# Kernel optimization log

Measured on AMD Instinct MI355X. Metric: run time of the kernel, lower is better.

Reference implementation:

```python
import jax, jax.numpy as jnp
import numpy as np

B, S, D, E, TOP_K = 4, 4096, 2048, 64, 2

def setup_inputs() -> dict:
    key = jax.random.key(0)
    k1, k2, k3, k4 = jax.random.split(key, 4)
    return {
        "mh_output": jax.random.normal(k1, (B, S, D), dtype=jnp.float32),
        "W_route": jax.random.normal(k2, (D, E), dtype=jnp.float32) * (1.0 / np.sqrt(D)),
        "b_route": jnp.zeros((E,), dtype=jnp.float32),
        "W_noise": jax.random.normal(k3, (D, E), dtype=jnp.float32) * (1.0 / np.sqrt(D)),
        "b_noise": jnp.zeros((E,), dtype=jnp.float32),
        "noise": jax.random.normal(k4, (B, S, E), dtype=jnp.float32),
    }

def reference(mh_output, W_route, b_route, W_noise, b_noise, noise):
    # logits / noise logits: [B, S, E]
    logits = jnp.einsum("bsd,de->bse", mh_output, W_route) + b_route
    noise_logits = jnp.einsum("bsd,de->bse", mh_output, W_noise) + b_noise
    noisy_logits = logits + noise * jax.nn.softplus(noise_logits)

    top_vals, indices = jax.lax.top_k(noisy_logits, TOP_K)  # [B,S,K]

    # scatter top-k values into a -inf-filled tensor, then softmax
    flat_vals = top_vals.reshape(-1, TOP_K)
    flat_idx = indices.reshape(-1, TOP_K)
    n_tok = flat_idx.shape[0]
    rows = jnp.arange(n_tok)[:, None]
    sparse = jnp.full((n_tok, E), -jnp.inf, dtype=noisy_logits.dtype)
    sparse = sparse.at[rows, flat_idx].set(flat_vals)
    probs = jax.nn.softmax(sparse, axis=-1).reshape(noisy_logits.shape)
    return probs, indices
```

## Files before the change

### kernel.cpp

```cpp
#include <hip/hip_runtime.h>
#include <math.h>

#define M_TOK 16384
#define D_DIM 2048
#define E_EXP 64
#define NCOL  128
#define BM    64
#define BK    64
#define NITER (D_DIM / BK)

typedef float  f32x4  __attribute__((ext_vector_type(4)));
typedef short  bf16x8 __attribute__((ext_vector_type(8)));

#define MFMA_B16(a, b, c) __builtin_amdgcn_mfma_f32_16x16x32_bf16((a), (b), (c), 0, 0, 0)

__device__ __forceinline__ unsigned short bfrne(float f) {
    unsigned int u = __float_as_uint(f);
    return (unsigned short)((u + 0x7fffu + ((u >> 16) & 1u)) >> 16);
}
__device__ __forceinline__ float bfhi(unsigned short h) {
    return __uint_as_float((unsigned int)h << 16);
}

__device__ __forceinline__ bool beats(double va, int ia, double vb, int ib) {
    return (va > vb) || (va == vb && ia < ib);
}

__device__ __forceinline__ void gload16(const void* g, void* lds) {
    __builtin_amdgcn_global_load_lds(
        (const __attribute__((address_space(1))) unsigned int*)g,
        (__attribute__((address_space(3))) unsigned int*)lds, 16, 0, 0);
}

__global__ __launch_bounds__(256) void prep_w(
    const float* __restrict__ Wr, const float* __restrict__ Wn,
    unsigned short* __restrict__ Wg)
{
    const int g    = blockIdx.x * 256 + threadIdx.x;
    const int lane = g & 63;
    const int cf   = (g >> 6) & 7;
    const int kblk = g >> 9;
    const int colL = (cf & 3) * 16 + (lane & 15);
    const float* __restrict__ W = (cf < 4) ? Wr : Wn;
    const int kbase = kblk * 32 + (lane >> 4) * 8;

    bf16x8 o0, o1, o2;
    #pragma unroll
    for (int j = 0; j < 8; ++j) {
        const float w = W[(size_t)(kbase + j) * E_EXP + colL];
        const unsigned short h0 = bfrne(w);
        const float r  = w - bfhi(h0);
        const unsigned short h1 = bfrne(r);
        const float r2 = r - bfhi(h1);
        const unsigned short h2 = bfrne(r2);
        o0[j] = (short)h0; o1[j] = (short)h1; o2[j] = (short)h2;
    }
    const size_t s0 = (((size_t)kblk * 3 + 0) * 8 + cf) * 64 + lane;
    const size_t s1 = (((size_t)kblk * 3 + 1) * 8 + cf) * 64 + lane;
    const size_t s2 = (((size_t)kblk * 3 + 2) * 8 + cf) * 64 + lane;
    *(bf16x8*)(Wg + s0 * 8) = o0;
    *(bf16x8*)(Wg + s1 * 8) = o1;
    *(bf16x8*)(Wg + s2 * 8) = o2;
}

__device__ __forceinline__ void load_b(const unsigned short* __restrict__ Wg,
                                       int it, int wc, int lane,
                                       bf16x8 (&Bv)[2][2][3])
{
    #pragma unroll
    for (int s = 0; s < 2; ++s) {
        const int kblk = it * 2 + s;
        #pragma unroll
        for (int cfi = 0; cfi < 2; ++cfi) {
            #pragma unroll
            for (int p = 0; p < 3; ++p) {
                const size_t idx = (((size_t)kblk * 3 + p) * 8 + (wc * 2 + cfi)) * 64 + lane;
                Bv[s][cfi][p] = *(const bf16x8*)(Wg + idx * 8);
            }
        }
    }
}

__device__ __forceinline__ void stage_a(const float* __restrict__ A, float* Alds,
                                        int buf, int k0, int tokBase, int tid)
{
    #pragma unroll
    for (int i = 0; i < 2; ++i) {
        const int c    = i * 512 + tid;
        const int tok  = c >> 4;
        const int off  = (c & 15) * 16;
        const int soff = off ^ ((tok & 7) << 4);
        const float* g = A + (size_t)(tokBase + tok) * D_DIM + k0 + (soff >> 2);
        char* l = (char*)Alds + buf * (BM * BK * 4) + i * 8192 + (tid >> 6) * 1024;
        gload16(g, l);
    }
}

__device__ __forceinline__ void split8(const float4& a, const float4& b,
                                       bf16x8& o0, bf16x8& o1, bf16x8& o2)
{
    const float v[8] = {a.x, a.y, a.z, a.w, b.x, b.y, b.z, b.w};
    #pragma unroll
    for (int j = 0; j < 8; ++j) {
        const unsigned short h0 = bfrne(v[j]);
        const float r  = v[j] - bfhi(h0);
        const unsigned short h1 = bfrne(r);
        const float r2 = r - bfhi(h1);
        const unsigned short h2 = bfrne(r2);
        o0[j] = (short)h0; o1[j] = (short)h1; o2[j] = (short)h2;
    }
}

__device__ __forceinline__ void compute_iter(const float* Abuf, int wr, int wc, int lane,
                                             const bf16x8 (&Bc)[2][2][3],
                                             f32x4 (&acch)[2][2], f32x4 (&accl)[2][2])
{
    const char* Ab = (const char*)Abuf;
    #pragma unroll
    for (int s = 0; s < 2; ++s) {
        bf16x8 a0[2], a1[2], a2[2];
        #pragma unroll
        for (int rf = 0; rf < 2; ++rf) {
            const int row  = wr * 32 + rf * 16 + (lane & 15);
            const int base = row * 256 + s * 128 + (lane >> 4) * 32;
            const int sw   = (row & 7) << 4;
            const float4 p = *(const float4*)(Ab + (base ^ sw));
            const float4 q = *(const float4*)(Ab + ((base + 16) ^ sw));
            split8(p, q, a0[rf], a1[rf], a2[rf]);
        }
        #pragma unroll
        for (int cfi = 0; cfi < 2; ++cfi) {
            #pragma unroll
            for (int rf = 0; rf < 2; ++rf) {
                acch[rf][cfi] = MFMA_B16(a0[rf], Bc[s][cfi][0], acch[rf][cfi]);
                accl[rf][cfi] = MFMA_B16(a0[rf], Bc[s][cfi][1], accl[rf][cfi]);
                accl[rf][cfi] = MFMA_B16(a1[rf], Bc[s][cfi][0], accl[rf][cfi]);
                accl[rf][cfi] = MFMA_B16(a1[rf], Bc[s][cfi][1], accl[rf][cfi]);
                accl[rf][cfi] = MFMA_B16(a0[rf], Bc[s][cfi][2], accl[rf][cfi]);
                accl[rf][cfi] = MFMA_B16(a2[rf], Bc[s][cfi][0], accl[rf][cfi]);
            }
        }
    }
}

__global__ __launch_bounds__(512, 2) void fused_router(
    const float* __restrict__ A,
    const unsigned short* __restrict__ Wg,
    const float* __restrict__ br, const float* __restrict__ bn,
    const float* __restrict__ noise,
    float* __restrict__ probs, float* __restrict__ idxo)
{
    __shared__ float Alds[2 * BM * BK];
    __shared__ float Llds[BM][NCOL + 1];

    const int tid  = threadIdx.x;
    const int lane = tid & 63;
    const int wid  = tid >> 6;
    const int wr   = wid >> 2;
    const int wc   = wid & 3;
    const int tokBase = blockIdx.x * BM;

    f32x4 acch[2][2], accl[2][2];
    const f32x4 zero4 = {0.f, 0.f, 0.f, 0.f};
    #pragma unroll
    for (int a = 0; a < 2; ++a)
        #pragma unroll
        for (int b = 0; b < 2; ++b) { acch[a][b] = zero4; accl[a][b] = zero4; }

    bf16x8 B0[2][2][3], B1[2][2][3];
    load_b(Wg, 0, wc, lane, B0);
    stage_a(A, Alds, 0, 0, tokBase, tid);
    asm volatile("s_waitcnt vmcnt(0)" ::: "memory");
    __syncthreads();

    #pragma unroll 1
    for (int it2 = 0; it2 < NITER / 2; ++it2) {
        const int ita = it2 * 2;
        const int itb = ita + 1;
        load_b(Wg, itb, wc, lane, B1);
        stage_a(A, Alds, 1, itb * BK, tokBase, tid);
        compute_iter(Alds, wr, wc, lane, B0, acch, accl);
        asm volatile("s_waitcnt vmcnt(0)" ::: "memory");
        __syncthreads();
        if (itb + 1 < NITER) {
            load_b(Wg, itb + 1, wc, lane, B0);
            stage_a(A, Alds, 0, (itb + 1) * BK, tokBase, tid);
        }
        compute_iter(Alds + BM * BK, wr, wc, lane, B1, acch, accl);
        asm volatile("s_waitcnt vmcnt(0)" ::: "memory");
        __syncthreads();
    }

    #pragma unroll
    for (int rf = 0; rf < 2; ++rf) {
        #pragma unroll
        for (int cfi = 0; cfi < 2; ++cfi) {
            const int col  = wc * 32 + cfi * 16 + (lane & 15);
            const int rowb = wr * 32 + rf * 16 + (lane >> 4) * 4;
            #pragma unroll
            for (int r = 0; r < 4; ++r)
                Llds[rowb + r][col] = acch[rf][cfi][r] + accl[rf][cfi][r];
        }
    }
    __syncthreads();

    const int token = tid >> 3;
    const int s8    = tid & 7;
    const int tokG  = tokBase + token;

    double v0 = -INFINITY, v1 = -INFINITY;
    int i0 = 0, i1 = 0;
    const float* nz = noise + (size_t)tokG * E_EXP + s8 * 8;
    #pragma unroll
    for (int j = 0; j < 8; ++j) {
        const int e = s8 * 8 + j;
        const double lg = (double)Llds[token][e]      + (double)br[e];
        const double nl = (double)Llds[token][64 + e] + (double)bn[e];
        const double sp = fmax(nl, 0.0) + log1p(exp(-fabs(nl)));
        const double v  = fma((double)nz[j], sp, lg);
        if (beats(v, e, v0, i0))      { v1 = v0; i1 = i0; v0 = v; i0 = e; }
        else if (beats(v, e, v1, i1)) { v1 = v;  i1 = e; }
    }
    #pragma unroll
    for (int m = 1; m < 8; m <<= 1) {
        const double w0 = __shfl_xor(v0, m), w1 = __shfl_xor(v1, m);
        const int    j0 = __shfl_xor(i0, m), j1 = __shfl_xor(i1, m);
        if (beats(v0, i0, w0, j0)) {
            if (!beats(v1, i1, w0, j0)) { v1 = w0; i1 = j0; }
        } else {
            if (beats(v0, i0, w1, j1)) { v1 = v0; i1 = i0; }
            else                       { v1 = w1; i1 = j1; }
            v0 = w0; i0 = j0;
        }
    }
    const double e1  = exp(v1 - v0);
    const double den = 1.0 + e1;
    const float p0 = (float)(1.0 / den);
    const float p1 = (float)(e1 / den);

    float out[8];
    #pragma unroll
    for (int j = 0; j < 8; ++j) {
        const int e = s8 * 8 + j;
        out[j] = (e == i0) ? p0 : ((e == i1) ? p1 : 0.0f);
    }
    float* pb = probs + (size_t)tokG * E_EXP + s8 * 8;
    *(float4*)(pb)     = make_float4(out[0], out[1], out[2], out[3]);
    *(float4*)(pb + 4) = make_float4(out[4], out[5], out[6], out[7]);
    if (s8 == 0)
        *(float2*)(idxo + (size_t)tokG * 2) = make_float2((float)i0, (float)i1);
}

extern "C" void kernel_launch(void* const* d_in, const int* in_sizes, int n_in,
                              void* d_out, int out_size, void* d_ws, size_t ws_size,
                              hipStream_t stream) {
    (void)in_sizes; (void)n_in; (void)out_size; (void)ws_size;
    const float* A  = (const float*)d_in[0];
    const float* Wr = (const float*)d_in[1];
    const float* br = (const float*)d_in[2];
    const float* Wn = (const float*)d_in[3];
    const float* bn = (const float*)d_in[4];
    const float* nz = (const float*)d_in[5];

    float* probs = (float*)d_out;
    float* idxo  = probs + (size_t)M_TOK * E_EXP;

    unsigned short* Wg = (unsigned short*)d_ws;

    prep_w<<<128, 256, 0, stream>>>(Wr, Wn, Wg);
    fused_router<<<M_TOK / BM, 512, 0, stream>>>(A, Wg, br, bn, nz, probs, idxo);
}
```

Before: 267.0 us.

## Split A to bf16 planes once at staging; register-prefetch A; fp32 epilogue

A tiles are now loaded into registers one iteration ahead, split into three bf16 planes once per element, and stored in padded LDS. Previously each wave re-split fp32 values read from LDS inside the compute loop, so the conversion repeated across waves. The old direct global-to-LDS loads are dropped, launch bounds go from two blocks per CU to one, and the routing epilogue switches from double to float math. The float epilogue is cheaper but risks top-k tie and ordering mismatches, and the lower occupancy may reduce latency hiding.

```diff
diff --git a/kernel.cpp b/kernel.cpp
--- a/kernel.cpp
+++ b/kernel.cpp
@@ -9,6 +9,11 @@
 #define BK    64
 #define NITER (D_DIM / BK)
 
+#define ROW_STRIDE 144
+#define PLANE (BM * ROW_STRIDE)
+#define BUFSZ (3 * PLANE)
+#define SMEM_BYTES (2 * BUFSZ)
+
 typedef float  f32x4  __attribute__((ext_vector_type(4)));
 typedef short  bf16x8 __attribute__((ext_vector_type(8)));
 
@@ -22,14 +27,8 @@
     return __uint_as_float((unsigned int)h << 16);
 }
 
-__device__ __forceinline__ bool beats(double va, int ia, double vb, int ib) {
+__device__ __forceinline__ bool beats(float va, int ia, float vb, int ib) {
     return (va > vb) || (va == vb && ia < ib);
-}
-
-__device__ __forceinline__ void gload16(const void* g, void* lds) {
-    __builtin_amdgcn_global_load_lds(
-        (const __attribute__((address_space(1))) unsigned int*)g,
-        (__attribute__((address_space(3))) unsigned int*)lds, 16, 0, 0);
 }
 
 __global__ __launch_bounds__(256) void prep_w(
@@ -81,19 +80,14 @@
     }
 }
 
-__device__ __forceinline__ void stage_a(const float* __restrict__ A, float* Alds,
-                                        int buf, int k0, int tokBase, int tid)
-{
-    #pragma unroll
-    for (int i = 0; i < 2; ++i) {
-        const int c    = i * 512 + tid;
-        const int tok  = c >> 4;
-        const int off  = (c & 15) * 16;
-        const int soff = off ^ ((tok & 7) << 4);
-        const float* g = A + (size_t)(tokBase + tok) * D_DIM + k0 + (soff >> 2);
-        char* l = (char*)Alds + buf * (BM * BK * 4) + i * 8192 + (tid >> 6) * 1024;
-        gload16(g, l);
-    }
+__device__ __forceinline__ void load_a(const float* __restrict__ A, int tokBase,
+                                       int it, int tid, float4& x, float4& y)
+{
+    const int row = tid >> 3;
+    const int kc8 = tid & 7;
+    const float* g = A + (size_t)(tokBase + row) * D_DIM + it * BK + kc8 * 8;
+    x = *(const float4*)(g);
+    y = *(const float4*)(g + 4);
 }
 
 __device__ __forceinline__ void split8(const float4& a, const float4& b,
@@ -111,22 +105,33 @@
     }
 }
 
-__device__ __forceinline__ void compute_iter(const float* Abuf, int wr, int wc, int lane,
+__device__ __forceinline__ void cvt_store(char* smem, int buf, int tid,
+                                          const float4& x, const float4& y)
+{
+    bf16x8 h0, h1, h2;
+    split8(x, y, h0, h1, h2);
+    const int row = tid >> 3;
+    const int kc8 = tid & 7;
+    char* base = smem + buf * BUFSZ + row * ROW_STRIDE + kc8 * 16;
+    *(bf16x8*)(base)             = h0;
+    *(bf16x8*)(base + PLANE)     = h1;
+    *(bf16x8*)(base + 2 * PLANE) = h2;
+}
+
+__device__ __forceinline__ void compute_iter(const char* Ab, int wr, int lane,
                                              const bf16x8 (&Bc)[2][2][3],
                                              f32x4 (&acch)[2][2], f32x4 (&accl)[2][2])
 {
-    const char* Ab = (const char*)Abuf;
     #pragma unroll
     for (int s = 0; s < 2; ++s) {
         bf16x8 a0[2], a1[2], a2[2];
         #pragma unroll
         for (int rf = 0; rf < 2; ++rf) {
-            const int row  = wr * 32 + rf * 16 + (lane & 15);
-            const int base = row * 256 + s * 128 + (lane >> 4) * 32;
-            const int sw   = (row & 7) << 4;
-            const float4 p = *(const float4*)(Ab + (base ^ sw));
-            const float4 q = *(const float4*)(Ab + ((base + 16) ^ sw));
-            split8(p, q, a0[rf], a1[rf], a2[rf]);
+            const int row = wr * 32 + rf * 16 + (lane & 15);
+            const int off = row * ROW_STRIDE + (s * 4 + (lane >> 4)) * 16;
+            a0[rf] = *(const bf16x8*)(Ab + off);
+            a1[rf] = *(const bf16x8*)(Ab + PLANE + off);
+            a2[rf] = *(const bf16x8*)(Ab + 2 * PLANE + off);
         }
         #pragma unroll
         for (int cfi = 0; cfi < 2; ++cfi) {
@@ -143,15 +148,14 @@
     }
 }
 
-__global__ __launch_bounds__(512, 2) void fused_router(
+__global__ __launch_bounds__(512, 1) void fused_router(
     const float* __restrict__ A,
     const unsigned short* __restrict__ Wg,
     const float* __restrict__ br, const float* __restrict__ bn,
     const float* __restrict__ noise,
     float* __restrict__ probs, float* __restrict__ idxo)
 {
-    __shared__ float Alds[2 * BM * BK];
-    __shared__ float Llds[BM][NCOL + 1];
+    __shared__ __align__(16) char smem[SMEM_BYTES];
 
     const int tid  = threadIdx.x;
     const int lane = tid & 63;
@@ -168,29 +172,33 @@
         for (int b = 0; b < 2; ++b) { acch[a][b] = zero4; accl[a][b] = zero4; }
 
     bf16x8 B0[2][2][3], B1[2][2][3];
+    float4 xE, yE, xO, yO;
+
+    load_a(A, tokBase, 0, tid, xE, yE);
     load_b(Wg, 0, wc, lane, B0);
-    stage_a(A, Alds, 0, 0, tokBase, tid);
-    asm volatile("s_waitcnt vmcnt(0)" ::: "memory");
+    load_a(A, tokBase, 1, tid, xO, yO);
+    cvt_store(smem, 0, tid, xE, yE);
     __syncthreads();
 
     #pragma unroll 1
     for (int it2 = 0; it2 < NITER / 2; ++it2) {
         const int ita = it2 * 2;
         const int itb = ita + 1;
+
         load_b(Wg, itb, wc, lane, B1);
-        stage_a(A, Alds, 1, itb * BK, tokBase, tid);
-        compute_iter(Alds, wr, wc, lane, B0, acch, accl);
-        asm volatile("s_waitcnt vmcnt(0)" ::: "memory");
+        cvt_store(smem, 1, tid, xO, yO);
+        if (ita + 2 < NITER) load_a(A, tokBase, ita + 2, tid, xE, yE);
+        compute_iter(smem, wr, lane, B0, acch, accl);
         __syncthreads();
-        if (itb + 1 < NITER) {
-            load_b(Wg, itb + 1, wc, lane, B0);
-            stage_a(A, Alds, 0, (itb + 1) * BK, tokBase, tid);
-        }
-        compute_iter(Alds + BM * BK, wr, wc, lane, B1, acch, accl);
-        asm volatile("s_waitcnt vmcnt(0)" ::: "memory");
+
+        if (itb + 1 < NITER) load_b(Wg, itb + 1, wc, lane, B0);
+        if (ita + 2 < NITER) cvt_store(smem, 0, tid, xE, yE);
+        if (itb + 2 < NITER) load_a(A, tokBase, itb + 2, tid, xO, yO);
+        compute_iter(smem + BUFSZ, wr, lane, B1, acch, accl);
         __syncthreads();
     }
 
+    float (*Llds)[NCOL + 1] = (float (*)[NCOL + 1])smem;
     #pragma unroll
     for (int rf = 0; rf < 2; ++rf) {
         #pragma unroll
@@ -208,23 +216,23 @@
     const int s8    = tid & 7;
     const int tokG  = tokBase + token;
 
-    double v0 = -INFINITY, v1 = -INFINITY;
+    float v0 = -INFINITY, v1 = -INFINITY;
     int i0 = 0, i1 = 0;
     const float* nz = noise + (size_t)tokG * E_EXP + s8 * 8;
     #pragma unroll
     for (int j = 0; j < 8; ++j) {
         const int e = s8 * 8 + j;
-        const double lg = (double)Llds[token][e]      + (double)br[e];
-        const double nl = (double)Llds[token][64 + e] + (double)bn[e];
-        const double sp = fmax(nl, 0.0) + log1p(exp(-fabs(nl)));
-        const double v  = fma((double)nz[j], sp, lg);
+        const float lg = Llds[token][e]      + br[e];
+        const float nl = Llds[token][64 + e] + bn[e];
+        const float sp = fmaxf(nl, 0.0f) + log1pf(expf(-fabsf(nl)));
+        const float v  = fmaf(nz[j], sp, lg);
         if (beats(v, e, v0, i0))      { v1 = v0; i1 = i0; v0 = v; i0 = e; }
         else if (beats(v, e, v1, i1)) { v1 = v;  i1 = e; }
     }
     #pragma unroll
     for (int m = 1; m < 8; m <<= 1) {
-        const double w0 = __shfl_xor(v0, m), w1 = __shfl_xor(v1, m);
-        const int    j0 = __shfl_xor(i0, m), j1 = __shfl_xor(i1, m);
+        const float w0 = __shfl_xor(v0, m), w1 = __shfl_xor(v1, m);
+        const int   j0 = __shfl_xor(i0, m), j1 = __shfl_xor(i1, m);
         if (beats(v0, i0, w0, j0)) {
             if (!beats(v1, i1, w0, j0)) { v1 = w0; i1 = j0; }
         } else {
@@ -233,10 +241,10 @@
             v0 = w0; i0 = j0;
         }
     }
-    const double e1  = exp(v1 - v0);
-    const double den = 1.0 + e1;
-    const float p0 = (float)(1.0 / den);
-    const float p1 = (float)(e1 / den);
+    const float e1  = expf(v1 - v0);
+    const float den = 1.0f + e1;
+    const float p0 = 1.0f / den;
+    const float p1 = e1 / den;
 
     float out[8];
     #pragma unroll
```

New measurement: 235.6 us. 11.7% less time.
